# Optimization experiments

Hardware: AMD Instinct MI355X
Metric: run time of the kernel (lower is better)

Reference implementation:

```python
import jax, jax.numpy as jnp
import numpy as np

N = 50000
E = 800000
IN_DIM = 512
HID = 256
LAT = 128
K = 10
ALPHA = 0.1
BN_EPS = 1e-5


def setup_inputs() -> dict:
    key = jax.random.key(0)
    ks = jax.random.split(key, 6)
    x = jax.random.normal(ks[0], (N, IN_DIM), dtype=jnp.float32)
    edge_index = jax.random.randint(ks[1], (2, E), 0, N, dtype=jnp.int64)
    W_proj = jax.random.normal(ks[2], (IN_DIM, LAT), dtype=jnp.float32) * (IN_DIM ** -0.5)
    W1 = jax.random.normal(ks[3], (LAT, HID), dtype=jnp.float32) * (LAT ** -0.5)
    W2 = jax.random.normal(ks[4], (HID, LAT), dtype=jnp.float32) * (HID ** -0.5)
    return {
        "x": x, "edge_index": edge_index, "W_proj": W_proj,
        "W1": W1, "b1": jnp.zeros((HID,), jnp.float32),
        "gamma1": jnp.ones((HID,), jnp.float32), "beta1": jnp.zeros((HID,), jnp.float32),
        "mean1": jnp.zeros((HID,), jnp.float32), "var1": jnp.ones((HID,), jnp.float32),
        "W2": W2, "b2": jnp.zeros((LAT,), jnp.float32),
        "gamma2": jnp.ones((LAT,), jnp.float32), "beta2": jnp.zeros((LAT,), jnp.float32),
        "mean2": jnp.zeros((LAT,), jnp.float32), "var2": jnp.ones((LAT,), jnp.float32),
    }


def _gcn_norm(edge_index, n):
    # add self-loops, symmetric normalization D^-1/2 A D^-1/2 (PyG gcn_norm)
    loops = jnp.arange(n, dtype=edge_index.dtype)
    src = jnp.concatenate([edge_index[0], loops])
    dst = jnp.concatenate([edge_index[1], loops])
    deg = jax.ops.segment_sum(jnp.ones_like(dst, jnp.float32), dst, num_segments=n)
    dinv = jax.lax.rsqrt(jnp.maximum(deg, 1.0))  # deg >= 1 with self-loops
    norm = dinv[src] * dinv[dst]
    return src, dst, norm


def _propagate(h, src, dst, norm, n):
    # gather -> scale -> scatter-add: out[dst] += norm * h[src]
    return jax.ops.segment_sum(h[src] * norm[:, None], dst, num_segments=n)


def _bn(h, gamma, beta, mean, var):
    # BatchNorm1d in eval mode (running stats)
    return (h - mean) * jax.lax.rsqrt(var + BN_EPS) * gamma + beta


def reference(x, edge_index, W_proj, W1, b1, gamma1, beta1, mean1, var1,
              W2, b2, gamma2, beta2, mean2, var2):
    n = x.shape[0]
    src, dst, norm = _gcn_norm(edge_index, n)

    z0 = x @ W_proj                                   # [N, LAT]
    h1 = _propagate(z0 @ W1, src, dst, norm, n) + b1  # GCNConv 1
    h1 = jax.nn.relu(_bn(h1, gamma1, beta1, mean1, var1))
    h2 = _propagate(h1 @ W2, src, dst, norm, n) + b2  # GCNConv 2
    h2 = jax.nn.relu(_bn(h2, gamma2, beta2, mean2, var2))

    # APPNP: h_k = (1-alpha) * A_hat h_{k-1} + alpha * h_0
    def step(h, _):
        h = (1.0 - ALPHA) * _propagate(h, src, dst, norm, n) + ALPHA * h2
        return h, None
    z_refined, _ = jax.lax.scan(step, h2, None, length=K)

    z = z_refined + z0
    row, col = edge_index[0], edge_index[1]
    adj = jax.nn.sigmoid(jnp.sum(z[row] * z[col], axis=1))  # [E]
    return adj, z
```

## Files before the change

kernel.cpp:

```cpp
#include <hip/hip_runtime.h>

#define N_NODES 50000
#define N_EDGES 800000
#define IN_DIM  512
#define HID     256
#define LAT     128
#define K_ITERS 10
#define BN_EPS  1e-5f

typedef __attribute__((ext_vector_type(8))) short bf16x8;
typedef __attribute__((ext_vector_type(4))) float f32x4;

__device__ inline float bflo(unsigned v) { return __builtin_bit_cast(float, v << 16); }
__device__ inline float bfhi(unsigned v) { return __builtin_bit_cast(float, v & 0xffff0000u); }
__device__ inline unsigned f2bf_bits(float f)
{
    unsigned u = __builtin_bit_cast(unsigned, f);
    return (u + 0x7fffu + ((u >> 16) & 1u)) >> 16;
}
__device__ inline unsigned packbf(float x, float y)
{
    return f2bf_bits(x) | (f2bf_bits(y) << 16);
}

__device__ inline void gload_lds16(const unsigned short* g, unsigned short* l)
{
    __builtin_amdgcn_global_load_lds(
        (const __attribute__((address_space(1))) unsigned int*)g,
        (__attribute__((address_space(3))) unsigned int*)l, 16, 0, 0);
}

__global__ void detect_dtype_kernel(const int* __restrict__ ei32, int* __restrict__ flag)
{
    __shared__ int any;
    if (threadIdx.x == 0) any = 0;
    __syncthreads();
    int local = 0;
    for (int i = threadIdx.x; i < 4096; i += blockDim.x)
        local |= ei32[2 * i + 1];
    if (local) atomicOr(&any, 1);
    __syncthreads();
    if (threadIdx.x == 0) flag[0] = (any != 0) ? 1 : 0;
}

__global__ void init_cnt_kernel(int* __restrict__ cnt, int n)
{
    int i = blockIdx.x * blockDim.x + threadIdx.x;
    if (i < n) cnt[i] = 1;
}

__global__ void convert_count_kernel(const void* __restrict__ ei, const int* __restrict__ flag,
                                     int* __restrict__ srcE, int* __restrict__ dstE,
                                     int* __restrict__ cnt, int E)
{
    int e = blockIdx.x * blockDim.x + threadIdx.x;
    if (e >= E) return;
    int s, d;
    if (*flag) {
        const int* p = (const int*)ei;
        s = p[e]; d = p[E + e];
    } else {
        const long long* p = (const long long*)ei;
        s = (int)p[e]; d = (int)p[E + e];
    }
    srcE[e] = s;
    dstE[e] = d;
    atomicAdd(&cnt[d], 1);
}

__global__ __launch_bounds__(256) void block_sum_kernel(const int* __restrict__ cnt,
                                                        int* __restrict__ bsum, int n)
{
    __shared__ int s[256];
    int i = blockIdx.x * 256 + threadIdx.x;
    s[threadIdx.x] = (i < n) ? cnt[i] : 0;
    __syncthreads();
    for (int off = 128; off > 0; off >>= 1) {
        if (threadIdx.x < off) s[threadIdx.x] += s[threadIdx.x + off];
        __syncthreads();
    }
    if (threadIdx.x == 0) bsum[blockIdx.x] = s[0];
}

__global__ __launch_bounds__(256) void block_scan_kernel(int* __restrict__ bsum, int nb)
{
    __shared__ int s[256];
    int t = threadIdx.x;
    int v = (t < nb) ? bsum[t] : 0;
    s[t] = v;
    __syncthreads();
    for (int off = 1; off < 256; off <<= 1) {
        int u = (t >= off) ? s[t - off] : 0;
        __syncthreads();
        s[t] += u;
        __syncthreads();
    }
    if (t < nb) bsum[t] = s[t] - v;
}

__global__ __launch_bounds__(256) void final_scan_kernel(const int* __restrict__ cnt,
                                                         const int* __restrict__ bsum,
                                                         int* __restrict__ rowoff,
                                                         int* __restrict__ cursor,
                                                         float* __restrict__ dinv, int n)
{
    __shared__ int s[256];
    int t = threadIdx.x;
    int i = blockIdx.x * 256 + t;
    int c = (i < n) ? cnt[i] : 0;
    s[t] = c;
    __syncthreads();
    for (int off = 1; off < 256; off <<= 1) {
        int u = (t >= off) ? s[t - off] : 0;
        __syncthreads();
        s[t] += u;
        __syncthreads();
    }
    if (i < n) {
        int excl = bsum[blockIdx.x] + s[t] - c;
        rowoff[i] = excl;
        cursor[i] = excl;
        dinv[i] = rsqrtf((float)c);
    }
    if (i == 0) rowoff[n] = N_EDGES + N_NODES;
}

__global__ void scatter_kernel(const int* __restrict__ srcE, const int* __restrict__ dstE,
                               const float* __restrict__ dinv, int* __restrict__ cursor,
                               unsigned* __restrict__ csr, int E, int n)
{
    int e = blockIdx.x * blockDim.x + threadIdx.x;
    if (e >= E + n) return;
    int s, d;
    if (e < E) { s = srcE[e]; d = dstE[e]; }
    else       { s = e - E;   d = s; }
    int pos = atomicAdd(&cursor[d], 1);
    float w = dinv[s] * dinv[d];
    csr[pos] = (unsigned)s | (f2bf_bits(w) << 16);
}

__global__ void transpose_cvt_tile(const float* __restrict__ in, unsigned short* __restrict__ out,
                                   int K, int C)
{
    int idx = blockIdx.x * 256 + threadIdx.x;
    if (idx >= K * C) return;
    int k = idx / C, col = idx - k * C;
    int dst = (col >> 7) * (K * 128) + (k >> 3) * 1024 + ((col & 127) << 3) + (k & 7);
    out[dst] = (unsigned short)f2bf_bits(in[idx]);
}

template<int KDIM, int EPI, bool AF32>
__global__ __launch_bounds__(256) void gemm_lds(const void* __restrict__ Ain,
                                                const unsigned short* __restrict__ Bt,
                                                unsigned short* __restrict__ Cout,
                                                int M, int Nc,
                                                const float* __restrict__ cb,
                                                const float* __restrict__ cg,
                                                const float* __restrict__ cbe,
                                                const float* __restrict__ cm,
                                                const float* __restrict__ cv)
{
    constexpr int BK = 64;
    constexpr int NC = KDIM / BK;
    __shared__ unsigned short Bl[2][BK * 128];
    const int tid  = threadIdx.x;
    const int wave = tid >> 6;
    const int lane = tid & 63;
    const int s  = lane & 15;
    const int kc = lane >> 4;
    const int wrow0   = blockIdx.y * 64 + wave * 16;
    const int colbase = blockIdx.x * 128;
    int arow = wrow0 + s; if (arow > M - 1) arow = M - 1;

    const float*          Af   = (const float*)Ain + (size_t)arow * KDIM + 8 * kc;
    const unsigned short* Ahp  = (const unsigned short*)Ain + (size_t)arow * KDIM + 8 * kc;
    const unsigned short* Bblk = Bt + (size_t)blockIdx.x * KDIM * 128;

    float4 Arf[2][2][2];
    bf16x8 Arh[2][2];
    f32x4  acc[8] = {};

    auto stage = [&](int c, int buf) {
#pragma unroll
        for (int i = 0; i < 4; ++i) {
            const int j = wave * 4 + i;
            gload_lds16(Bblk + (size_t)c * 8192 + j * 512 + lane * 8, &Bl[buf][j * 512]);
        }
    };

    stage(0, 0);
#pragma unroll
    for (int kk = 0; kk < 2; ++kk) {
        if constexpr (AF32) {
            Arf[0][kk][0] = *(const float4*)(Af + 32 * kk);
            Arf[0][kk][1] = *(const float4*)(Af + 32 * kk + 4);
        } else {
            Arh[0][kk] = *(const bf16x8*)(Ahp + 32 * kk);
        }
    }
    __syncthreads();

#pragma unroll
    for (int c = 0; c < NC; ++c) {
        if (c + 1 < NC) {
            stage(c + 1, (c + 1) & 1);
#pragma unroll
            for (int kk = 0; kk < 2; ++kk) {
                if constexpr (AF32) {
                    Arf[(c + 1) & 1][kk][0] = *(const float4*)(Af + (c + 1) * 64 + 32 * kk);
                    Arf[(c + 1) & 1][kk][1] = *(const float4*)(Af + (c + 1) * 64 + 32 * kk + 4);
                } else {
                    Arh[(c + 1) & 1][kk] = *(const bf16x8*)(Ahp + (c + 1) * 64 + 32 * kk);
                }
            }
        }
#pragma unroll
        for (int kk = 0; kk < 2; ++kk) {
            bf16x8 af;
            if constexpr (AF32) {
                float4 u0 = Arf[c & 1][kk][0];
                float4 u1 = Arf[c & 1][kk][1];
                af[0] = (short)f2bf_bits(u0.x); af[1] = (short)f2bf_bits(u0.y);
                af[2] = (short)f2bf_bits(u0.z); af[3] = (short)f2bf_bits(u0.w);
                af[4] = (short)f2bf_bits(u1.x); af[5] = (short)f2bf_bits(u1.y);
                af[6] = (short)f2bf_bits(u1.z); af[7] = (short)f2bf_bits(u1.w);
            } else {
                af = Arh[c & 1][kk];
            }
#pragma unroll
            for (int t = 0; t < 8; ++t) {
                bf16x8 bf = *(const bf16x8*)&Bl[c & 1][((kk * 4 + kc) * 128 + t * 16 + s) * 8];
                acc[t] = __builtin_amdgcn_mfma_f32_16x16x32_bf16(af, bf, acc[t], 0, 0, 0);
            }
        }
        __syncthreads();
    }

#pragma unroll
    for (int t = 0; t < 8; ++t) {
        const int col = colbase + t * 16 + s;
        float sc = 1.f, sh = 0.f;
        if (EPI == 1) {
            sc = cg[col] * rsqrtf(cv[col] + BN_EPS);
            sh = (cb[col] - cm[col]) * sc + cbe[col];
        }
#pragma unroll
        for (int j = 0; j < 4; ++j) {
            const int crow = wrow0 + kc * 4 + j;
            if (crow < M) {
                float xv = acc[t][j];
                if (EPI == 1) xv = fmaxf(fmaf(xv, sc, sh), 0.f);
                Cout[(size_t)crow * Nc + col] = (unsigned short)f2bf_bits(xv);
            }
        }
    }
}

template<int MODE>
__global__ __launch_bounds__(256) void prop_row(const unsigned* __restrict__ in,
                                                const int* __restrict__ rowoff,
                                                const unsigned* __restrict__ csr,
                                                const unsigned* __restrict__ h2h,
                                                const unsigned* __restrict__ z0h,
                                                float* __restrict__ outf,
                                                unsigned* __restrict__ outh,
                                                const float* __restrict__ bb,
                                                const float* __restrict__ bg,
                                                const float* __restrict__ bbe,
                                                const float* __restrict__ bm,
                                                const float* __restrict__ bv)
{
    const int node = blockIdx.x * 4 + (threadIdx.x >> 6);
    const int lane = threadIdx.x & 63;
    const int g = lane >> 4, s = lane & 15;
    const int e0 = rowoff[node], e1 = rowoff[node + 1];

    float f[8] = {};
    int e = e0 + g;
    while (e < e1) {
        unsigned P[6];
        uint4 V[6];
#pragma unroll
        for (int i = 0; i < 6; ++i) { P[i] = 0; V[i] = make_uint4(0u, 0u, 0u, 0u); }
#pragma unroll
        for (int i = 0; i < 6; ++i)
            if (e + 4 * i < e1) P[i] = csr[e + 4 * i];
#pragma unroll
        for (int i = 0; i < 6; ++i)
            if (e + 4 * i < e1) V[i] = *(const uint4*)&in[(size_t)(P[i] & 0xFFFFu) * 64 + 4 * s];
#pragma unroll
        for (int i = 0; i < 6; ++i) {
            const float w = __builtin_bit_cast(float, P[i] & 0xffff0000u);
            f[0] = fmaf(w, bflo(V[i].x), f[0]); f[1] = fmaf(w, bfhi(V[i].x), f[1]);
            f[2] = fmaf(w, bflo(V[i].y), f[2]); f[3] = fmaf(w, bfhi(V[i].y), f[3]);
            f[4] = fmaf(w, bflo(V[i].z), f[4]); f[5] = fmaf(w, bfhi(V[i].z), f[5]);
            f[6] = fmaf(w, bflo(V[i].w), f[6]); f[7] = fmaf(w, bfhi(V[i].w), f[7]);
        }
        e += 24;
    }
#pragma unroll
    for (int i = 0; i < 8; ++i) {
        f[i] += __shfl_xor(f[i], 16, 64);
        f[i] += __shfl_xor(f[i], 32, 64);
    }

    if (g == 0) {
        const size_t o = (size_t)node * 64 + 4 * s;
        uint4 ov;
        if (MODE == 0) {
            ov.x = packbf(f[0], f[1]); ov.y = packbf(f[2], f[3]);
            ov.z = packbf(f[4], f[5]); ov.w = packbf(f[6], f[7]);
            *(uint4*)&outh[o] = ov;
        } else if (MODE == 1) {
            float4 G0 = *(const float4*)&bg[8 * s],  G1 = *(const float4*)&bg[8 * s + 4];
            float4 V0 = *(const float4*)&bv[8 * s],  V1 = *(const float4*)&bv[8 * s + 4];
            float4 B0 = *(const float4*)&bb[8 * s],  B1 = *(const float4*)&bb[8 * s + 4];
            float4 M0 = *(const float4*)&bm[8 * s],  M1 = *(const float4*)&bm[8 * s + 4];
            float4 E0 = *(const float4*)&bbe[8 * s], E1 = *(const float4*)&bbe[8 * s + 4];
            float gg[8] = {G0.x, G0.y, G0.z, G0.w, G1.x, G1.y, G1.z, G1.w};
            float vv[8] = {V0.x, V0.y, V0.z, V0.w, V1.x, V1.y, V1.z, V1.w};
            float bbv[8] = {B0.x, B0.y, B0.z, B0.w, B1.x, B1.y, B1.z, B1.w};
            float mm[8] = {M0.x, M0.y, M0.z, M0.w, M1.x, M1.y, M1.z, M1.w};
            float ee[8] = {E0.x, E0.y, E0.z, E0.w, E1.x, E1.y, E1.z, E1.w};
            float r[8];
#pragma unroll
            for (int i = 0; i < 8; ++i) {
                float sc = gg[i] * rsqrtf(vv[i] + BN_EPS);
                float sh = (bbv[i] - mm[i]) * sc + ee[i];
                r[i] = fmaxf(fmaf(f[i], sc, sh), 0.f);
            }
            ov.x = packbf(r[0], r[1]); ov.y = packbf(r[2], r[3]);
            ov.z = packbf(r[4], r[5]); ov.w = packbf(r[6], r[7]);
            *(uint4*)&outh[o] = ov;
        } else if (MODE == 2) {
            uint4 hv = *(const uint4*)&h2h[o];
            ov.x = packbf(fmaf(0.9f, f[0], 0.1f * bflo(hv.x)), fmaf(0.9f, f[1], 0.1f * bfhi(hv.x)));
            ov.y = packbf(fmaf(0.9f, f[2], 0.1f * bflo(hv.y)), fmaf(0.9f, f[3], 0.1f * bfhi(hv.y)));
            ov.z = packbf(fmaf(0.9f, f[4], 0.1f * bflo(hv.z)), fmaf(0.9f, f[5], 0.1f * bfhi(hv.z)));
            ov.w = packbf(fmaf(0.9f, f[6], 0.1f * bflo(hv.w)), fmaf(0.9f, f[7], 0.1f * bfhi(hv.w)));
            *(uint4*)&outh[o] = ov;
        } else {
            uint4 hv = *(const uint4*)&h2h[o];
            uint4 zv = *(const uint4*)&z0h[o];
            float r[8];
            r[0] = fmaf(0.9f, f[0], 0.1f * bflo(hv.x)) + bflo(zv.x);
            r[1] = fmaf(0.9f, f[1], 0.1f * bfhi(hv.x)) + bfhi(zv.x);
            r[2] = fmaf(0.9f, f[2], 0.1f * bflo(hv.y)) + bflo(zv.y);
            r[3] = fmaf(0.9f, f[3], 0.1f * bfhi(hv.y)) + bfhi(zv.y);
            r[4] = fmaf(0.9f, f[4], 0.1f * bflo(hv.z)) + bflo(zv.z);
            r[5] = fmaf(0.9f, f[5], 0.1f * bfhi(hv.z)) + bfhi(zv.z);
            r[6] = fmaf(0.9f, f[6], 0.1f * bflo(hv.w)) + bflo(zv.w);
            r[7] = fmaf(0.9f, f[7], 0.1f * bfhi(hv.w)) + bfhi(zv.w);
            *(float4*)&outf[(size_t)node * LAT + 8 * s]     = make_float4(r[0], r[1], r[2], r[3]);
            *(float4*)&outf[(size_t)node * LAT + 8 * s + 4] = make_float4(r[4], r[5], r[6], r[7]);
            ov.x = packbf(r[0], r[1]); ov.y = packbf(r[2], r[3]);
            ov.z = packbf(r[4], r[5]); ov.w = packbf(r[6], r[7]);
            *(uint4*)&outh[o] = ov;
        }
    }
}

__global__ __launch_bounds__(256) void edge_dot_mfma(const unsigned* __restrict__ zh,
                                                     const int* __restrict__ srcE,
                                                     const int* __restrict__ dstE,
                                                     float* __restrict__ adj)
{
    const int gw = blockIdx.x * 4 + (threadIdx.x >> 6);
    const int base = gw * 16;
    const int lane = threadIdx.x & 63;
    const int s = lane & 15, kc = lane >> 4;
    const int r = srcE[base + s];
    const int c = dstE[base + s];
    const unsigned* zr = &zh[(size_t)r * 64 + 4 * kc];
    const unsigned* zc = &zh[(size_t)c * 64 + 4 * kc];
    f32x4 acc = {};
#pragma unroll
    for (int k0 = 0; k0 < 4; ++k0) {
        bf16x8 af = *(const bf16x8*)(zr + 16 * k0);
        bf16x8 bf = *(const bf16x8*)(zc + 16 * k0);
        acc = __builtin_amdgcn_mfma_f32_16x16x32_bf16(af, bf, acc, 0, 0, 0);
    }
    if ((s >> 2) == kc) {
        const int j = s & 3;
        float v = (j == 0) ? acc[0] : (j == 1) ? acc[1] : (j == 2) ? acc[2] : acc[3];
        adj[base + s] = 1.f / (1.f + expf(-v));
    }
}

extern "C" void kernel_launch(void* const* d_in, const int* in_sizes, int n_in,
                              void* d_out, int out_size, void* d_ws, size_t ws_size,
                              hipStream_t stream)
{
    const float* x     = (const float*)d_in[0];
    const void*  ei    = d_in[1];
    const float* Wproj = (const float*)d_in[2];
    const float* W1    = (const float*)d_in[3];
    const float* b1    = (const float*)d_in[4];
    const float* g1    = (const float*)d_in[5];
    const float* be1   = (const float*)d_in[6];
    const float* m1    = (const float*)d_in[7];
    const float* v1    = (const float*)d_in[8];
    const float* W2    = (const float*)d_in[9];
    const float* b2    = (const float*)d_in[10];
    const float* g2    = (const float*)d_in[11];
    const float* be2   = (const float*)d_in[12];
    const float* m2    = (const float*)d_in[13];
    const float* v2    = (const float*)d_in[14];

    float* out_adj = (float*)d_out;
    float* out_z   = (float*)d_out + N_EDGES;

    char* w = (char*)d_ws;
    size_t off = 0;
    auto alloc = [&](size_t bytes) {
        void* p = w + off;
        off += (bytes + 255) & ~(size_t)255;
        return p;
    };
    const size_t NB = (size_t)N_NODES * 64 * 4;
    const int NBLK = (N_NODES + 255) / 256;

    int*            flag   = (int*)           alloc(4);
    int*            cnt    = (int*)           alloc((size_t)N_NODES * 4);
    int*            cursor = (int*)           alloc((size_t)N_NODES * 4);
    int*            rowoff = (int*)           alloc((size_t)(N_NODES + 1) * 4);
    float*          dinv   = (float*)         alloc((size_t)N_NODES * 4);
    int*            bsum   = (int*)           alloc(256 * 4);
    int*            srcE   = (int*)           alloc((size_t)N_EDGES * 4);
    int*            dstE   = (int*)           alloc((size_t)N_EDGES * 4);
    unsigned*       csr    = (unsigned*)      alloc((size_t)(N_EDGES + N_NODES) * 4);
    unsigned short* Wpt    = (unsigned short*)alloc((size_t)LAT * IN_DIM * 2);
    unsigned short* W1t    = (unsigned short*)alloc((size_t)HID * LAT * 2);
    unsigned short* W2t    = (unsigned short*)alloc((size_t)LAT * HID * 2);
    unsigned*       z0h    = (unsigned*)      alloc(NB);
    unsigned*       p0h    = (unsigned*)      alloc(NB);
    unsigned short* h1h    = (unsigned short*)alloc(2 * NB);
    unsigned*       t2h    = (unsigned*)      alloc(NB);
    unsigned*       h2h    = (unsigned*)      alloc(NB);

    unsigned* pingA = (unsigned*)h1h;
    unsigned* pingB = (unsigned*)h1h + N_NODES * 64;

    detect_dtype_kernel<<<1, 256, 0, stream>>>((const int*)ei, flag);
    init_cnt_kernel<<<(N_NODES + 255) / 256, 256, 0, stream>>>(cnt, N_NODES);
    convert_count_kernel<<<(N_EDGES + 255) / 256, 256, 0, stream>>>(ei, flag, srcE, dstE, cnt, N_EDGES);
    block_sum_kernel<<<NBLK, 256, 0, stream>>>(cnt, bsum, N_NODES);
    block_scan_kernel<<<1, 256, 0, stream>>>(bsum, NBLK);
    final_scan_kernel<<<NBLK, 256, 0, stream>>>(cnt, bsum, rowoff, cursor, dinv, N_NODES);
    scatter_kernel<<<(N_EDGES + N_NODES + 255) / 256, 256, 0, stream>>>(srcE, dstE, dinv, cursor,
                                                                        csr, N_EDGES, N_NODES);

    transpose_cvt_tile<<<(IN_DIM * LAT + 255) / 256, 256, 0, stream>>>(Wproj, Wpt, IN_DIM, LAT);
    transpose_cvt_tile<<<(LAT * HID + 255) / 256, 256, 0, stream>>>(W1, W1t, LAT, HID);
    transpose_cvt_tile<<<(HID * LAT + 255) / 256, 256, 0, stream>>>(W2, W2t, HID, LAT);

    const int gy = (N_NODES + 63) / 64;
    const int pgrid = N_NODES / 4;

    gemm_lds<IN_DIM, 0, true><<<dim3(1, gy), 256, 0, stream>>>(x, Wpt, (unsigned short*)z0h,
                                                               N_NODES, LAT,
                                                               nullptr, nullptr, nullptr, nullptr, nullptr);
    prop_row<0><<<pgrid, 256, 0, stream>>>(z0h, rowoff, csr, nullptr, nullptr, nullptr, p0h,
                                           nullptr, nullptr, nullptr, nullptr, nullptr);
    gemm_lds<LAT, 1, false><<<dim3(2, gy), 256, 0, stream>>>(p0h, W1t, h1h, N_NODES, HID,
                                                             b1, g1, be1, m1, v1);
    gemm_lds<HID, 0, false><<<dim3(1, gy), 256, 0, stream>>>(h1h, W2t, (unsigned short*)t2h,
                                                             N_NODES, LAT,
                                                             nullptr, nullptr, nullptr, nullptr, nullptr);
    prop_row<1><<<pgrid, 256, 0, stream>>>(t2h, rowoff, csr, nullptr, nullptr, nullptr, h2h,
                                           b2, g2, be2, m2, v2);

    const unsigned* cur = h2h;
    for (int it = 0; it < K_ITERS; ++it) {
        if (it == K_ITERS - 1) {
            prop_row<3><<<pgrid, 256, 0, stream>>>(cur, rowoff, csr, h2h, z0h, out_z, z0h,
                                                   nullptr, nullptr, nullptr, nullptr, nullptr);
        } else {
            unsigned* nxt = (it & 1) ? pingB : pingA;
            prop_row<2><<<pgrid, 256, 0, stream>>>(cur, rowoff, csr, h2h, nullptr, nullptr, nxt,
                                                   nullptr, nullptr, nullptr, nullptr, nullptr);
            cur = nxt;
        }
    }

    edge_dot_mfma<<<N_EDGES / 64, 256, 0, stream>>>(z0h, srcE, dstE, out_adj);
}
```

Measured before the change: 638.8 us.

## Split propagation feature dimension into two halves across blocks with nontemporal memory ops

The propagation kernel now splits each node's 128-dim bf16 row into two 64-dim halves, each handled by a separate block, so the grid doubles. Each wave uses 8 edge groups of 8 lanes instead of 4 groups of 16, with 3 edges in flight per lane, and adds one more shuffle stage to the reduction. CSR loads, residual loads and output stores are switched to nontemporal hints. The aim is more parallelism and memory-level concurrency per node, at the cost of reading the CSR and row offsets twice and possibly reducing L2 reuse of the gathered rows.

```diff
diff --git a/kernel.cpp b/kernel.cpp
--- a/kernel.cpp
+++ b/kernel.cpp
@@ -10,6 +10,7 @@
 
 typedef __attribute__((ext_vector_type(8))) short bf16x8;
 typedef __attribute__((ext_vector_type(4))) float f32x4;
+typedef __attribute__((ext_vector_type(4))) unsigned u32x4;
 
 __device__ inline float bflo(unsigned v) { return __builtin_bit_cast(float, v << 16); }
 __device__ inline float bfhi(unsigned v) { return __builtin_bit_cast(float, v & 0xffff0000u); }
@@ -257,39 +258,44 @@
 }
 
 template<int MODE>
-__global__ __launch_bounds__(256) void prop_row(const unsigned* __restrict__ in,
-                                                const int* __restrict__ rowoff,
-                                                const unsigned* __restrict__ csr,
-                                                const unsigned* __restrict__ h2h,
-                                                const unsigned* __restrict__ z0h,
-                                                float* __restrict__ outf,
-                                                unsigned* __restrict__ outh,
-                                                const float* __restrict__ bb,
-                                                const float* __restrict__ bg,
-                                                const float* __restrict__ bbe,
-                                                const float* __restrict__ bm,
-                                                const float* __restrict__ bv)
-{
-    const int node = blockIdx.x * 4 + (threadIdx.x >> 6);
+__global__ __launch_bounds__(256) void prop_half(const unsigned* __restrict__ in,
+                                                 const int* __restrict__ rowoff,
+                                                 const unsigned* __restrict__ csr,
+                                                 const unsigned* __restrict__ h2h,
+                                                 const unsigned* __restrict__ z0h,
+                                                 float* __restrict__ outf,
+                                                 unsigned* __restrict__ outh,
+                                                 const float* __restrict__ bb,
+                                                 const float* __restrict__ bg,
+                                                 const float* __restrict__ bbe,
+                                                 const float* __restrict__ bm,
+                                                 const float* __restrict__ bv)
+{
+    const int NHB  = N_NODES / 4;
+    const int half = (blockIdx.x >= NHB) ? 1 : 0;
+    const int nb   = half ? (blockIdx.x - NHB) : blockIdx.x;
+    const int wave = threadIdx.x >> 6;
     const int lane = threadIdx.x & 63;
-    const int g = lane >> 4, s = lane & 15;
+    const int node = nb * 4 + wave;
+    const int j = lane >> 3, c = lane & 7;
     const int e0 = rowoff[node], e1 = rowoff[node + 1];
+    const int hoff = half * 32 + c * 4;
 
     float f[8] = {};
-    int e = e0 + g;
+    int e = e0 + j;
     while (e < e1) {
-        unsigned P[6];
-        uint4 V[6];
-#pragma unroll
-        for (int i = 0; i < 6; ++i) { P[i] = 0; V[i] = make_uint4(0u, 0u, 0u, 0u); }
-#pragma unroll
-        for (int i = 0; i < 6; ++i)
-            if (e + 4 * i < e1) P[i] = csr[e + 4 * i];
-#pragma unroll
-        for (int i = 0; i < 6; ++i)
-            if (e + 4 * i < e1) V[i] = *(const uint4*)&in[(size_t)(P[i] & 0xFFFFu) * 64 + 4 * s];
-#pragma unroll
-        for (int i = 0; i < 6; ++i) {
+        unsigned P[3];
+        u32x4 V[3];
+#pragma unroll
+        for (int i = 0; i < 3; ++i) { P[i] = 0; V[i] = (u32x4){0u, 0u, 0u, 0u}; }
+#pragma unroll
+        for (int i = 0; i < 3; ++i)
+            if (e + 8 * i < e1) P[i] = __builtin_nontemporal_load(&csr[e + 8 * i]);
+#pragma unroll
+        for (int i = 0; i < 3; ++i)
+            if (e + 8 * i < e1) V[i] = *(const u32x4*)&in[(size_t)(P[i] & 0xFFFFu) * 64 + hoff];
+#pragma unroll
+        for (int i = 0; i < 3; ++i) {
             const float w = __builtin_bit_cast(float, P[i] & 0xffff0000u);
             f[0] = fmaf(w, bflo(V[i].x), f[0]); f[1] = fmaf(w, bfhi(V[i].x), f[1]);
             f[2] = fmaf(w, bflo(V[i].y), f[2]); f[3] = fmaf(w, bfhi(V[i].y), f[3]);
@@ -300,23 +306,25 @@
     }
 #pragma unroll
     for (int i = 0; i < 8; ++i) {
+        f[i] += __shfl_xor(f[i], 8, 64);
         f[i] += __shfl_xor(f[i], 16, 64);
         f[i] += __shfl_xor(f[i], 32, 64);
     }
 
-    if (g == 0) {
-        const size_t o = (size_t)node * 64 + 4 * s;
-        uint4 ov;
+    if (j == 0) {
+        const size_t o = (size_t)node * 64 + hoff;
+        const int d0 = half * 64 + c * 8;
+        u32x4 ov;
         if (MODE == 0) {
             ov.x = packbf(f[0], f[1]); ov.y = packbf(f[2], f[3]);
             ov.z = packbf(f[4], f[5]); ov.w = packbf(f[6], f[7]);
-            *(uint4*)&outh[o] = ov;
+            __builtin_nontemporal_store(ov, (u32x4*)&outh[o]);
         } else if (MODE == 1) {
-            float4 G0 = *(const float4*)&bg[8 * s],  G1 = *(const float4*)&bg[8 * s + 4];
-            float4 V0 = *(const float4*)&bv[8 * s],  V1 = *(const float4*)&bv[8 * s + 4];
-            float4 B0 = *(const float4*)&bb[8 * s],  B1 = *(const float4*)&bb[8 * s + 4];
-            float4 M0 = *(const float4*)&bm[8 * s],  M1 = *(const float4*)&bm[8 * s + 4];
-            float4 E0 = *(const float4*)&bbe[8 * s], E1 = *(const float4*)&bbe[8 * s + 4];
+            float4 G0 = *(const float4*)&bg[d0],  G1 = *(const float4*)&bg[d0 + 4];
+            float4 V0 = *(const float4*)&bv[d0],  V1 = *(const float4*)&bv[d0 + 4];
+            float4 B0 = *(const float4*)&bb[d0],  B1 = *(const float4*)&bb[d0 + 4];
+            float4 M0 = *(const float4*)&bm[d0],  M1 = *(const float4*)&bm[d0 + 4];
+            float4 E0 = *(const float4*)&bbe[d0], E1 = *(const float4*)&bbe[d0 + 4];
             float gg[8] = {G0.x, G0.y, G0.z, G0.w, G1.x, G1.y, G1.z, G1.w};
             float vv[8] = {V0.x, V0.y, V0.z, V0.w, V1.x, V1.y, V1.z, V1.w};
             float bbv[8] = {B0.x, B0.y, B0.z, B0.w, B1.x, B1.y, B1.z, B1.w};
@@ -331,17 +339,17 @@
             }
             ov.x = packbf(r[0], r[1]); ov.y = packbf(r[2], r[3]);
             ov.z = packbf(r[4], r[5]); ov.w = packbf(r[6], r[7]);
-            *(uint4*)&outh[o] = ov;
+            __builtin_nontemporal_store(ov, (u32x4*)&outh[o]);
         } else if (MODE == 2) {
-            uint4 hv = *(const uint4*)&h2h[o];
+            u32x4 hv = __builtin_nontemporal_load((const u32x4*)&h2h[o]);
             ov.x = packbf(fmaf(0.9f, f[0], 0.1f * bflo(hv.x)), fmaf(0.9f, f[1], 0.1f * bfhi(hv.x)));
             ov.y = packbf(fmaf(0.9f, f[2], 0.1f * bflo(hv.y)), fmaf(0.9f, f[3], 0.1f * bfhi(hv.y)));
             ov.z = packbf(fmaf(0.9f, f[4], 0.1f * bflo(hv.z)), fmaf(0.9f, f[5], 0.1f * bfhi(hv.z)));
             ov.w = packbf(fmaf(0.9f, f[6], 0.1f * bflo(hv.w)), fmaf(0.9f, f[7], 0.1f * bfhi(hv.w)));
-            *(uint4*)&outh[o] = ov;
+            __builtin_nontemporal_store(ov, (u32x4*)&outh[o]);
         } else {
-            uint4 hv = *(const uint4*)&h2h[o];
-            uint4 zv = *(const uint4*)&z0h[o];
+            u32x4 hv = __builtin_nontemporal_load((const u32x4*)&h2h[o]);
+            u32x4 zv = __builtin_nontemporal_load((const u32x4*)&z0h[o]);
             float r[8];
             r[0] = fmaf(0.9f, f[0], 0.1f * bflo(hv.x)) + bflo(zv.x);
             r[1] = fmaf(0.9f, f[1], 0.1f * bfhi(hv.x)) + bfhi(zv.x);
@@ -351,11 +359,13 @@
             r[5] = fmaf(0.9f, f[5], 0.1f * bfhi(hv.z)) + bfhi(zv.z);
             r[6] = fmaf(0.9f, f[6], 0.1f * bflo(hv.w)) + bflo(zv.w);
             r[7] = fmaf(0.9f, f[7], 0.1f * bfhi(hv.w)) + bfhi(zv.w);
-            *(float4*)&outf[(size_t)node * LAT + 8 * s]     = make_float4(r[0], r[1], r[2], r[3]);
-            *(float4*)&outf[(size_t)node * LAT + 8 * s + 4] = make_float4(r[4], r[5], r[6], r[7]);
+            f32x4 o0 = {r[0], r[1], r[2], r[3]};
+            f32x4 o1 = {r[4], r[5], r[6], r[7]};
+            __builtin_nontemporal_store(o0, (f32x4*)&outf[(size_t)node * LAT + d0]);
+            __builtin_nontemporal_store(o1, (f32x4*)&outf[(size_t)node * LAT + d0 + 4]);
             ov.x = packbf(r[0], r[1]); ov.y = packbf(r[2], r[3]);
             ov.z = packbf(r[4], r[5]); ov.w = packbf(r[6], r[7]);
-            *(uint4*)&outh[o] = ov;
+            __builtin_nontemporal_store(ov, (u32x4*)&outh[o]);
         }
     }
 }
@@ -455,30 +465,30 @@
     transpose_cvt_tile<<<(HID * LAT + 255) / 256, 256, 0, stream>>>(W2, W2t, HID, LAT);
 
     const int gy = (N_NODES + 63) / 64;
-    const int pgrid = N_NODES / 4;
+    const int pgrid = 2 * (N_NODES / 4);
 
     gemm_lds<IN_DIM, 0, true><<<dim3(1, gy), 256, 0, stream>>>(x, Wpt, (unsigned short*)z0h,
                                                                N_NODES, LAT,
                                                                nullptr, nullptr, nullptr, nullptr, nullptr);
-    prop_row<0><<<pgrid, 256, 0, stream>>>(z0h, rowoff, csr, nullptr, nullptr, nullptr, p0h,
-                                           nullptr, nullptr, nullptr, nullptr, nullptr);
+    prop_half<0><<<pgrid, 256, 0, stream>>>(z0h, rowoff, csr, nullptr, nullptr, nullptr, p0h,
+                                            nullptr, nullptr, nullptr, nullptr, nullptr);
     gemm_lds<LAT, 1, false><<<dim3(2, gy), 256, 0, stream>>>(p0h, W1t, h1h, N_NODES, HID,
                                                              b1, g1, be1, m1, v1);
     gemm_lds<HID, 0, false><<<dim3(1, gy), 256, 0, stream>>>(h1h, W2t, (unsigned short*)t2h,
                                                              N_NODES, LAT,
                                                              nullptr, nullptr, nullptr, nullptr, nullptr);
-    prop_row<1><<<pgrid, 256, 0, stream>>>(t2h, rowoff, csr, nullptr, nullptr, nullptr, h2h,
-                                           b2, g2, be2, m2, v2);
+    prop_half<1><<<pgrid, 256, 0, stream>>>(t2h, rowoff, csr, nullptr, nullptr, nullptr, h2h,
+                                            b2, g2, be2, m2, v2);
 
     const unsigned* cur = h2h;
     for (int it = 0; it < K_ITERS; ++it) {
         if (it == K_ITERS - 1) {
-            prop_row<3><<<pgrid, 256, 0, stream>>>(cur, rowoff, csr, h2h, z0h, out_z, z0h,
-                                                   nullptr, nullptr, nullptr, nullptr, nullptr);
+            prop_half<3><<<pgrid, 256, 0, stream>>>(cur, rowoff, csr, h2h, z0h, out_z, z0h,
+                                                    nullptr, nullptr, nullptr, nullptr, nullptr);
         } else {
             unsigned* nxt = (it & 1) ? pingB : pingA;
-            prop_row<2><<<pgrid, 256, 0, stream>>>(cur, rowoff, csr, h2h, nullptr, nullptr, nxt,
-                                                   nullptr, nullptr, nullptr, nullptr, nullptr);
+            prop_half<2><<<pgrid, 256, 0, stream>>>(cur, rowoff, csr, h2h, nullptr, nullptr, nxt,
+                                                    nullptr, nullptr, nullptr, nullptr, nullptr);
             cur = nxt;
         }
     }
```

Result: slower. 830.8 us (+30.1%).
